# Optimization experiments

Measured on AMD Instinct MI355X. Metric: run time of the kernel, lower is better.

## Reference

```python
import jax, jax.numpy as jnp
import numpy as np

EMBED_DIM = 64
N_NODES = 1024
LEAKY_SLOPE = 0.01  # torch.nn.LeakyReLU default


def setup_inputs() -> dict:
    key = jax.random.key(0)
    ks = jax.random.split(key, 7)
    F = EMBED_DIM
    emb = jax.random.normal(ks[0], (2, N_NODES, F), dtype=jnp.float32)
    # MLP params (stored as (in, out) so y = x @ W + b)
    W1 = jax.random.normal(ks[1], (2 * F, F), dtype=jnp.float32) / np.sqrt(2 * F)
    b1 = jnp.zeros((F,), dtype=jnp.float32)
    W2 = jax.random.normal(ks[2], (F, F // 2), dtype=jnp.float32) / np.sqrt(F)
    b2 = jnp.zeros((F // 2,), dtype=jnp.float32)
    W3 = jax.random.normal(ks[3], (F // 2, 1), dtype=jnp.float32) / np.sqrt(F // 2)
    b3 = jnp.zeros((1,), dtype=jnp.float32)
    return {"embeddings": emb, "W1": W1, "b1": b1, "W2": W2, "b2": b2, "W3": W3, "b3": b3}


def reference(embeddings, W1, b1, W2, b2, W3, b3):
    B, N, F = embeddings.shape
    # Pairwise concat without explicit repeat: instead of building [B,N,N,2F]
    # then one GEMM, split W1 into the left-half and right-half contributions
    # (concat([a,b]) @ W1 == a @ W1[:F] + b @ W1[F:]), computed on [B,N,F]
    # then broadcast-added -> avoids the 2F concat materialization.
    left = embeddings @ W1[:F]    # [B, N, F_out] contribution of node i
    right = embeddings @ W1[F:]   # [B, N, F_out] contribution of node j
    h = left[:, :, None, :] + right[:, None, :, :] + b1  # [B, N, N, F]
    h = jax.nn.leaky_relu(h, LEAKY_SLOPE)
    h = jax.nn.leaky_relu(h @ W2 + b2, LEAKY_SLOPE)       # [B, N, N, F/2]
    out = (h @ W3 + b3)[..., 0]                           # [B, N, N]
    return out
```

## Files before the change

### kernel.cpp

```cpp
#include <hip/hip_runtime.h>
#include <hip/hip_bf16.h>
#include <hip/hip_fp16.h>

#define NNODES 1024
#define FDIM   64
#define KOUT   32

typedef _Float16 f16x8 __attribute__((ext_vector_type(8)));
typedef _Float16 f16x4 __attribute__((ext_vector_type(4)));
typedef __fp16   fp16x2 __attribute__((ext_vector_type(2)));
typedef float    f32x4  __attribute__((ext_vector_type(4)));
typedef float    f32x16 __attribute__((ext_vector_type(16)));

__global__ __launch_bounds__(256, 4) void fused_pair_mlp(
    const float* __restrict__ emb, const float* __restrict__ W1,
    const float* __restrict__ b1,
    const float* __restrict__ W2, const float* __restrict__ b2,
    const float* __restrict__ W3, const float* __restrict__ b3,
    float* __restrict__ out)
{
    const int tid  = threadIdx.x;
    const int wv   = tid >> 6;
    const int ln   = tid & 63;
    const int ln16 = ln & 15;
    const int grp  = (ln >> 4) & 3;
    const int j32  = ln & 31;
    const int hh   = ln >> 5;

    const int b  = blockIdx.z;
    const int j0 = blockIdx.x * 32;
    const int i0 = blockIdx.y * 32;

    __shared__ _Float16 semb[64][72];
    __shared__ _Float16 lleft[32][64];
    __shared__ _Float16 rtile[32][72];

    {
        const float* ebase = emb + (size_t)b * NNODES * FDIM;
#pragma unroll
        for (int q = 0; q < 4; ++q) {
            const int idx  = q * 256 + tid;
            const int row  = idx >> 4;
            const int c4   = idx & 15;
            const int grow = (row < 32) ? (i0 + row) : (j0 + row - 32);
            const float4 v = *(const float4*)(ebase + (size_t)grow * FDIM + c4 * 4);
            f16x4 hv = { (_Float16)v.x, (_Float16)v.y, (_Float16)v.z, (_Float16)v.w };
            *(f16x4*)(&semb[row][c4 * 4]) = hv;
        }
    }

    const int ow = wv * 16 + ln16;
    f16x8 bW1L[2], bW1R[2];
#pragma unroll
    for (int s = 0; s < 2; ++s)
#pragma unroll
        for (int e = 0; e < 8; ++e) {
            bW1L[s][e] = (_Float16)W1[(s * 32 + grp * 8 + e) * FDIM + ow];
            bW1R[s][e] = (_Float16)W1[(64 + s * 32 + grp * 8 + e) * FDIM + ow];
        }
    const float b1v = b1[ow];

    f16x8 aW2[4];
#pragma unroll
    for (int t = 0; t < 4; ++t)
#pragma unroll
        for (int e = 0; e < 8; ++e)
            aW2[t][e] = (_Float16)W2[(t * 16 + hh * 8 + e) * KOUT + j32];

    f16x8 a3[2];
#pragma unroll
    for (int t = 0; t < 2; ++t)
#pragma unroll
        for (int e = 0; e < 8; ++e)
            a3[t][e] = (_Float16)W3[(e & 3) + 8 * (e >> 2) + 16 * t + 4 * hh];

    f32x16 cinit;
#pragma unroll
    for (int r = 0; r < 16; ++r)
        cinit[r] = b2[(r & 3) + 8 * (r >> 2) + 4 * hh];
    f32x16 c3;
    const float bias3 = b3[0];
#pragma unroll
    for (int r = 0; r < 16; ++r)
        c3[r] = bias3;

    __syncthreads();

#pragma unroll
    for (int mt = 0; mt < 2; ++mt) {
        const _Float16* ap = &semb[mt * 16 + ln16][grp * 8];
        const f16x8 a0 = *(const f16x8*)ap;
        const f16x8 a1 = *(const f16x8*)(ap + 32);
        f32x4 acc = {0.f, 0.f, 0.f, 0.f};
        acc = __builtin_amdgcn_mfma_f32_16x16x32_f16(a0, bW1L[0], acc, 0, 0, 0);
        acc = __builtin_amdgcn_mfma_f32_16x16x32_f16(a1, bW1L[1], acc, 0, 0, 0);
#pragma unroll
        for (int r = 0; r < 4; ++r)
            lleft[mt * 16 + grp * 4 + r][ow] = (_Float16)(acc[r] + b1v);
    }
#pragma unroll
    for (int mt = 0; mt < 2; ++mt) {
        const _Float16* ap = &semb[32 + mt * 16 + ln16][grp * 8];
        const f16x8 a0 = *(const f16x8*)ap;
        const f16x8 a1 = *(const f16x8*)(ap + 32);
        f32x4 acc = {0.f, 0.f, 0.f, 0.f};
        acc = __builtin_amdgcn_mfma_f32_16x16x32_f16(a0, bW1R[0], acc, 0, 0, 0);
        acc = __builtin_amdgcn_mfma_f32_16x16x32_f16(a1, bW1R[1], acc, 0, 0, 0);
#pragma unroll
        for (int r = 0; r < 4; ++r)
            rtile[mt * 16 + grp * 4 + r][ow] = (_Float16)acc[r];
    }

    __syncthreads();

    f16x8 rj[4];
#pragma unroll
    for (int t = 0; t < 4; ++t)
        rj[t] = *(const f16x8*)(&rtile[j32][t * 16 + hh * 8]);

    const _Float16 slope = (_Float16)0.01f;
    float pprev = 0.f;

#pragma unroll 2
    for (int q = 0; q < 8; ++q) {
        const int ii = wv * 8 + q;
        const _Float16* lrow = &lleft[ii][0];

        f32x16 acc = cinit;
#pragma unroll
        for (int t = 0; t < 4; ++t) {
            const f16x8 l = *(const f16x8*)(lrow + t * 16 + hh * 8);
            f16x8 x = l + rj[t];
            x = __builtin_elementwise_max(x, x * slope);
            acc = __builtin_amdgcn_mfma_f32_32x32x16_f16(aW2[t], x, acc, 0, 0, 0);
        }

        f16x8 pb0, pb1;
#pragma unroll
        for (int e = 0; e < 4; ++e) {
            const fp16x2 t0 = __builtin_amdgcn_cvt_pkrtz(acc[2 * e], acc[2 * e + 1]);
            pb0[2 * e] = (_Float16)t0[0]; pb0[2 * e + 1] = (_Float16)t0[1];
            const fp16x2 t1 = __builtin_amdgcn_cvt_pkrtz(acc[8 + 2 * e], acc[9 + 2 * e]);
            pb1[2 * e] = (_Float16)t1[0]; pb1[2 * e + 1] = (_Float16)t1[1];
        }
        pb0 = __builtin_elementwise_max(pb0, pb0 * slope);
        pb1 = __builtin_elementwise_max(pb1, pb1 * slope);

        f32x16 d = c3;
        d = __builtin_amdgcn_mfma_f32_32x32x16_f16(a3[0], pb0, d, 0, 0, 0);
        d = __builtin_amdgcn_mfma_f32_32x32x16_f16(a3[1], pb1, d, 0, 0, 0);
        const float p = d[0];

        if (q & 1) {
            const float v   = hh ? p : pprev;
            const int   row = i0 + wv * 8 + (q - 1) + hh;
            out[((size_t)b * NNODES + row) * NNODES + j0 + j32] = v;
        } else {
            pprev = p;
        }
    }
}

extern "C" void kernel_launch(void* const* d_in, const int* in_sizes, int n_in,
                              void* d_out, int out_size, void* d_ws, size_t ws_size,
                              hipStream_t stream) {
    const float* emb = (const float*)d_in[0];
    const float* W1  = (const float*)d_in[1];
    const float* b1  = (const float*)d_in[2];
    const float* W2  = (const float*)d_in[3];
    const float* b2  = (const float*)d_in[4];
    const float* W3  = (const float*)d_in[5];
    const float* b3  = (const float*)d_in[6];
    float* out = (float*)d_out;
    (void)d_ws; (void)ws_size;

    fused_pair_mlp<<<dim3(NNODES / 32, NNODES / 32, 2), dim3(256), 0, stream>>>(
        emb, W1, b1, W2, b2, W3, b3, out);
}
```

Measured before the change: 26.48 us.

## Widen j-tile per block and replace final MFMA with fp32 leaky-ReLU dot

Each block now covers 32 i rows by 128 j columns, with each wave owning 32 j columns and looping over all 32 i rows. This amortizes the W1 projection of the i-side embeddings and the per-block setup over more output pairs. The third layer no longer packs to fp16 and runs two MFMAs. It computes leaky_relu(x)·w3 in fp32 as 0.505·Σw·x + 0.495·Σw·|x|, then combines the two half-waves with a cross-lane shuffle. This keeps the third layer in fp32 instead of fp16 and drops the cvt/pack work, but adds 32 FMAs per lane per i row. The grid shrinks by 4x and the launch_bounds occupancy hint is removed.

After: 24.61 us. 1.08x faster.

```diff
diff --git a/kernel.cpp b/kernel.cpp
--- a/kernel.cpp
+++ b/kernel.cpp
@@ -5,14 +5,15 @@
 #define NNODES 1024
 #define FDIM   64
 #define KOUT   32
+#define NJ     128
+#define NI     32
 
 typedef _Float16 f16x8 __attribute__((ext_vector_type(8)));
 typedef _Float16 f16x4 __attribute__((ext_vector_type(4)));
-typedef __fp16   fp16x2 __attribute__((ext_vector_type(2)));
 typedef float    f32x4  __attribute__((ext_vector_type(4)));
 typedef float    f32x16 __attribute__((ext_vector_type(16)));
 
-__global__ __launch_bounds__(256, 4) void fused_pair_mlp(
+__global__ __launch_bounds__(256) void fused_pair_mlp(
     const float* __restrict__ emb, const float* __restrict__ W1,
     const float* __restrict__ b1,
     const float* __restrict__ W2, const float* __restrict__ b2,
@@ -28,21 +29,21 @@
     const int hh   = ln >> 5;
 
     const int b  = blockIdx.z;
-    const int j0 = blockIdx.x * 32;
-    const int i0 = blockIdx.y * 32;
+    const int j0 = blockIdx.x * NJ;
+    const int i0 = blockIdx.y * NI;
 
-    __shared__ _Float16 semb[64][72];
-    __shared__ _Float16 lleft[32][64];
-    __shared__ _Float16 rtile[32][72];
+    __shared__ _Float16 semb[160][72];
+    __shared__ _Float16 lleft[NI][64];
+    __shared__ _Float16 rtile[NJ][72];
 
     {
         const float* ebase = emb + (size_t)b * NNODES * FDIM;
 #pragma unroll
-        for (int q = 0; q < 4; ++q) {
+        for (int q = 0; q < 10; ++q) {
             const int idx  = q * 256 + tid;
             const int row  = idx >> 4;
             const int c4   = idx & 15;
-            const int grow = (row < 32) ? (i0 + row) : (j0 + row - 32);
+            const int grow = (row < NI) ? (i0 + row) : (j0 + row - NI);
             const float4 v = *(const float4*)(ebase + (size_t)grow * FDIM + c4 * 4);
             f16x4 hv = { (_Float16)v.x, (_Float16)v.y, (_Float16)v.z, (_Float16)v.w };
             *(f16x4*)(&semb[row][c4 * 4]) = hv;
@@ -67,22 +68,15 @@
         for (int e = 0; e < 8; ++e)
             aW2[t][e] = (_Float16)W2[(t * 16 + hh * 8 + e) * KOUT + j32];
 
-    f16x8 a3[2];
+    f32x16 cinit;
+    float  w3f[16];
 #pragma unroll
-    for (int t = 0; t < 2; ++t)
-#pragma unroll
-        for (int e = 0; e < 8; ++e)
-            a3[t][e] = (_Float16)W3[(e & 3) + 8 * (e >> 2) + 16 * t + 4 * hh];
-
-    f32x16 cinit;
-#pragma unroll
-    for (int r = 0; r < 16; ++r)
-        cinit[r] = b2[(r & 3) + 8 * (r >> 2) + 4 * hh];
-    f32x16 c3;
+    for (int r = 0; r < 16; ++r) {
+        const int k2 = (r & 3) + 8 * (r >> 2) + 4 * hh;
+        cinit[r] = b2[k2];
+        w3f[r]   = W3[k2];
+    }
     const float bias3 = b3[0];
-#pragma unroll
-    for (int r = 0; r < 16; ++r)
-        c3[r] = bias3;
 
     __syncthreads();
 
@@ -99,8 +93,8 @@
             lleft[mt * 16 + grp * 4 + r][ow] = (_Float16)(acc[r] + b1v);
     }
 #pragma unroll
-    for (int mt = 0; mt < 2; ++mt) {
-        const _Float16* ap = &semb[32 + mt * 16 + ln16][grp * 8];
+    for (int mt = 0; mt < 8; ++mt) {
+        const _Float16* ap = &semb[NI + mt * 16 + ln16][grp * 8];
         const f16x8 a0 = *(const f16x8*)ap;
         const f16x8 a1 = *(const f16x8*)(ap + 32);
         f32x4 acc = {0.f, 0.f, 0.f, 0.f};
@@ -116,14 +110,14 @@
     f16x8 rj[4];
 #pragma unroll
     for (int t = 0; t < 4; ++t)
-        rj[t] = *(const f16x8*)(&rtile[j32][t * 16 + hh * 8]);
+        rj[t] = *(const f16x8*)(&rtile[wv * 32 + j32][t * 16 + hh * 8]);
 
     const _Float16 slope = (_Float16)0.01f;
+    const int jj = j0 + wv * 32 + j32;
     float pprev = 0.f;
 
 #pragma unroll 2
-    for (int q = 0; q < 8; ++q) {
-        const int ii = wv * 8 + q;
+    for (int ii = 0; ii < NI; ++ii) {
         const _Float16* lrow = &lleft[ii][0];
 
         f32x16 acc = cinit;
@@ -135,26 +129,20 @@
             acc = __builtin_amdgcn_mfma_f32_32x32x16_f16(aW2[t], x, acc, 0, 0, 0);
         }
 
-        f16x8 pb0, pb1;
+        float pa = 0.f, pb = 0.f;
 #pragma unroll
-        for (int e = 0; e < 4; ++e) {
-            const fp16x2 t0 = __builtin_amdgcn_cvt_pkrtz(acc[2 * e], acc[2 * e + 1]);
-            pb0[2 * e] = (_Float16)t0[0]; pb0[2 * e + 1] = (_Float16)t0[1];
-            const fp16x2 t1 = __builtin_amdgcn_cvt_pkrtz(acc[8 + 2 * e], acc[9 + 2 * e]);
-            pb1[2 * e] = (_Float16)t1[0]; pb1[2 * e + 1] = (_Float16)t1[1];
+        for (int r = 0; r < 16; ++r) {
+            pa = fmaf(w3f[r], acc[r],        pa);
+            pb = fmaf(w3f[r], fabsf(acc[r]), pb);
         }
-        pb0 = __builtin_elementwise_max(pb0, pb0 * slope);
-        pb1 = __builtin_elementwise_max(pb1, pb1 * slope);
+        float p = fmaf(0.505f, pa, 0.495f * pb);
+        p += __shfl_xor(p, 32, 64);
+        p += bias3;
 
-        f32x16 d = c3;
-        d = __builtin_amdgcn_mfma_f32_32x32x16_f16(a3[0], pb0, d, 0, 0, 0);
-        d = __builtin_amdgcn_mfma_f32_32x32x16_f16(a3[1], pb1, d, 0, 0, 0);
-        const float p = d[0];
-
-        if (q & 1) {
+        if (ii & 1) {
             const float v   = hh ? p : pprev;
-            const int   row = i0 + wv * 8 + (q - 1) + hh;
-            out[((size_t)b * NNODES + row) * NNODES + j0 + j32] = v;
+            const int   row = i0 + (ii - 1) + hh;
+            out[((size_t)b * NNODES + row) * NNODES + jj] = v;
         } else {
             pprev = p;
         }
@@ -174,6 +162,6 @@
     float* out = (float*)d_out;
     (void)d_ws; (void)ws_size;
 
-    fused_pair_mlp<<<dim3(NNODES / 32, NNODES / 32, 2), dim3(256), 0, stream>>>(
+    fused_pair_mlp<<<dim3(NNODES / NJ, NNODES / NI, 2), dim3(256), 0, stream>>>(
         emb, W1, b1, W2, b2, W3, b3, out);
 }
```
